# Kernel optimization log

Measured on AMD Instinct MI355X. Metric: run time of the kernel, lower is better.

## Reference

```python
import jax, jax.numpy as jnp
import numpy as np
from jax import lax

EPS = 1e-06
QP_ITERS = 500  # unrolled mirror-descent iterations for the simplex QP


def mlp_embed(x, W1, b1, W2, b2):
    # embedding_net: 2-layer MLP, [B, N, in_dim] -> [B, N, embed_dim]
    h = jax.nn.relu(jnp.einsum('bni,ih->bnh', x, W1) + b1)
    return jnp.einsum('bnh,hd->bnd', h, W2) + b2


def batch_svdd(emb, eps):
    # emb: [B, S, D].  SVDD dual QP per task:
    #   min_a  a^T K a - diag(K)^T a   s.t.  a >= 0, sum(a) = 1
    # (Q = 2K, p = -diag(K), G = -I, h = 0, A = 1^T, b = 1 in the torch QPFunction call)
    B, S, D = emb.shape
    K = jnp.einsum('bsd,btd->bst', emb, emb) + eps * jnp.eye(S, dtype=emb.dtype)
    kdiag = jnp.diagonal(K, axis1=-2, axis2=-1)  # [B, S]
    # Solve on the simplex with exponentiated-gradient (mirror descent with KL),
    # which converges to the unique QP optimum (K is PD after the eps jitter).
    # Per-task step size from the Gershgorin bound: eta <= 1 / (2 * ||K||_inf).
    eta = 1.0 / (2.0 * jnp.max(jnp.sum(jnp.abs(K), axis=-1), axis=-1, keepdims=True))  # [B,1]
    a0 = jnp.full((B, S), 1.0 / S, dtype=emb.dtype)

    def step(a, _):
        g = 2.0 * jnp.einsum('bst,bt->bs', K, a) - kdiag  # grad of a^T K a - kdiag^T a
        a = jax.nn.softmax(jnp.log(a + 1e-30) - eta * g, axis=-1)
        return a, None

    alphas, _ = lax.scan(step, a0, None, length=QP_ITERS)
    centers = jnp.einsum('bs,bsd->bd', alphas, emb)  # sum(alphas * inputs, dim=1)
    return centers


def setup_inputs() -> dict:
    key = jax.random.key(0)
    ks = jax.random.split(key, 4)
    tasks, shot, n_query, in_dim, hid, emb = 256, 32, 64, 1024, 2048, 512
    support_inputs = jax.random.normal(ks[0], (tasks, shot, in_dim), jnp.float32)
    query_inputs = jax.random.normal(ks[1], (tasks, n_query, in_dim), jnp.float32)
    W1 = jax.random.normal(ks[2], (in_dim, hid), jnp.float32) / np.sqrt(in_dim)
    b1 = jnp.zeros((hid,), jnp.float32)
    W2 = jax.random.normal(ks[3], (hid, emb), jnp.float32) / np.sqrt(hid)
    b2 = jnp.zeros((emb,), jnp.float32)
    return {'support_inputs': support_inputs, 'query_inputs': query_inputs,
            'W1': W1, 'b1': b1, 'W2': W2, 'b2': b2}


def reference(support_inputs, query_inputs, W1, b1, W2, b2):
    support_emb = mlp_embed(support_inputs, W1, b1, W2, b2)  # [B, S, D]
    centers = batch_svdd(support_emb, EPS)                   # [B, D]
    query_emb = mlp_embed(query_inputs, W1, b1, W2, b2)      # [B, Q, D]
    logits = -jnp.sum((centers[:, None, :] - query_emb) ** 2, axis=-1)  # [B, Q]
    return logits
```

## Files before the change

### kernel.cpp

```cpp
#include <hip/hip_runtime.h>
#include <hip/hip_bf16.h>

typedef __attribute__((ext_vector_type(8))) short bf16x8;
typedef __attribute__((ext_vector_type(4))) float f32x4;
typedef __attribute__((ext_vector_type(4))) unsigned short us4;

__device__ __forceinline__ unsigned short bf16_rne(float f) {
  unsigned u = __float_as_uint(f);
  unsigned r = u + 0x7fffu + ((u >> 16) & 1u);
  return (unsigned short)(r >> 16);
}

__device__ __forceinline__ void gload16(const void* g, void* l) {
  typedef const __attribute__((address_space(1))) unsigned int* gas;
  typedef __attribute__((address_space(3))) unsigned int* las;
  __builtin_amdgcn_global_load_lds((gas)g, (las)l, 16, 0, 0);
}

__device__ __forceinline__ float lane_f(float v, int l) {
  return __int_as_float(__builtin_amdgcn_readlane(__float_as_int(v), l));
}

template <int CTRL>
__device__ __forceinline__ float dpp_add(float x) {
  return x + __int_as_float(__builtin_amdgcn_update_dpp(0, __float_as_int(x), CTRL, 0xf, 0xf, true));
}

#define BAR() asm volatile("s_barrier" ::: "memory")
#define VMCNT0() asm volatile("s_waitcnt vmcnt(0)" ::: "memory")
#define LGKM4() asm volatile("s_waitcnt lgkmcnt(4)" ::: "memory")
#define LGKM0() asm volatile("s_waitcnt lgkmcnt(0)" ::: "memory")
#define SB() __builtin_amdgcn_sched_barrier(0)

__global__ __launch_bounds__(256) void castx(const float* __restrict__ sup,
                                             const float* __restrict__ qry,
                                             unsigned short* __restrict__ X) {
  const int stride = gridDim.x * blockDim.x;
  for (int i = blockIdx.x * blockDim.x + threadIdx.x; i < 6291456; i += stride) {
    float4 v = (i < 2097152) ? ((const float4*)sup)[i] : ((const float4*)qry)[i - 2097152];
    us4 o = { bf16_rne(v.x), bf16_rne(v.y), bf16_rne(v.z), bf16_rne(v.w) };
    *(us4*)(X + (size_t)i * 4) = o;
  }
}

__global__ __launch_bounds__(256) void transcast(const float* __restrict__ src,
                                                 unsigned short* __restrict__ dst,
                                                 int R, int C) {
  __shared__ float t[32][33];
  const int tx = threadIdx.x & 31, ty = threadIdx.x >> 5;
  const int c0 = blockIdx.x * 32, r0 = blockIdx.y * 32;
#pragma unroll
  for (int j = 0; j < 4; j++)
    t[ty + j * 8][tx] = src[(size_t)(r0 + ty + j * 8) * C + c0 + tx];
  __syncthreads();
#pragma unroll
  for (int j = 0; j < 4; j++)
    dst[(size_t)(c0 + ty + j * 8) * R + r0 + tx] = bf16_rne(t[tx][ty + j * 8]);
}

#define MFMA_Q(AO, BO, MOFF, NOFF)                                                  \
  __builtin_amdgcn_s_setprio(1);                                                    \
  _Pragma("unroll") for (int i_ = 0; i_ < 4; ++i_)                                  \
  _Pragma("unroll") for (int j_ = 0; j_ < 2; ++j_)                                  \
  _Pragma("unroll") for (int ks_ = 0; ks_ < 2; ++ks_)                               \
    acc[(MOFF) + i_][(NOFF) + j_] = __builtin_amdgcn_mfma_f32_16x16x32_bf16(        \
        AO[i_][ks_], BO[j_][ks_], acc[(MOFF) + i_][(NOFF) + j_], 0, 0, 0);          \
  __builtin_amdgcn_s_setprio(0);

#define RDA(KS, ACH, MH, I) \
  (*(const bf16x8*)(lsc + ((ACH) * 32768 + (MH) * 8192 + (I) * 2048) + ((KS) ? vA_1 : vA_0)))
#define RDB(KS, BCH, JI) \
  (*(const bf16x8*)(lsc + ((BCH) * 32768 + (JI) * 2048) + ((KS) ? vB_1 : vB_0)))

#define STG(GLP, CHOFF, HALF)                                                     \
  gload16((GLP) + (size_t)((HALF) * 128) * ld,                                    \
          (char*)ls + ((CHOFF) + (HALF) * 16384) + wid * 1024);                   \
  gload16((GLP) + (size_t)((HALF) * 128 + 64) * ld,                               \
          (char*)ls + ((CHOFF) + (HALF) * 16384 + 8192) + wid * 1024);

#define TILE(ACH, BCH, ASO, BSO, T)                                               \
  {                                                                               \
    VMCNT0();                                                                     \
    BAR();                                                                        \
    _Pragma("unroll") for (int i = 0; i < 4; ++i) {                               \
      afr[i][0] = RDA(0, ACH, 0, i); afr[i][1] = RDA(1, ACH, 0, i);               \
    }                                                                             \
    _Pragma("unroll") for (int j = 0; j < 2; ++j) {                               \
      bfr0[j][0] = RDB(0, BCH, j); bfr0[j][1] = RDB(1, BCH, j);                   \
    }                                                                             \
    _Pragma("unroll") for (int j = 0; j < 2; ++j) {                               \
      bfr1[j][0] = RDB(0, BCH, 2 + j); bfr1[j][1] = RDB(1, BCH, 2 + j);           \
    }                                                                             \
    const char* Ap_ = AgL + (size_t)(T) * 128;                                    \
    const char* Bp_ = BgL + (size_t)(T) * 128;                                    \
    STG(Ap_, ASO, 0); STG(Ap_, ASO, 1);                                           \
    STG(Bp_, BSO, 0); STG(Bp_, BSO, 1);                                           \
    LGKM4(); SB();                                                                \
    MFMA_Q(afr, bfr0, 0, 0);                                                      \
    LGKM0(); SB();                                                                \
    MFMA_Q(afr, bfr1, 0, 2);                                                      \
    _Pragma("unroll") for (int i = 0; i < 4; ++i) {                               \
      afr[i][0] = RDA(0, ACH, 1, i); afr[i][1] = RDA(1, ACH, 1, i);               \
    }                                                                             \
    LGKM0(); SB();                                                                \
    MFMA_Q(afr, bfr1, 4, 2);                                                      \
    MFMA_Q(afr, bfr0, 4, 0);                                                      \
  }

template <int ACT, int OUTBF>
__global__ __launch_bounds__(512) void gemm256(const unsigned short* __restrict__ A,
                                               const unsigned short* __restrict__ BT,
                                               const float* __restrict__ bias,
                                               void* __restrict__ Cout,
                                               int M, int N, int K) {
  __shared__ __attribute__((aligned(16))) short ls[4][16384];
  const int tid = threadIdx.x, lane = tid & 63, wid = tid >> 6;
  const int wm = wid >> 2, wn = wid & 3;
  const int l15 = lane & 15, lg = lane >> 4;

  int lin = blockIdx.y * gridDim.x + blockIdx.x;
  int nwg = gridDim.x * gridDim.y;
  int swz = (lin & 7) * (nwg >> 3) + (lin >> 3);
  int bx = swz % gridDim.x, by = swz / gridDim.x;
  const int m0 = by * 256, n0 = bx * 256;

  const size_t ld = (size_t)K * 2;
  const char* Ag = (const char*)A + (size_t)m0 * ld;
  const char* Bg = (const char*)BT + (size_t)n0 * ld;
  const int NT = K >> 6;
  const char* lsc = (const char*)ls;

  const int swz4 = (l15 & 7) << 4;
  const int bk0 = (l15 * 128 + lg * 16) ^ swz4;
  const int bk1 = (l15 * 128 + 64 + lg * 16) ^ swz4;
  const int vA_0 = bk0 + wm * 16384, vA_1 = bk1 + wm * 16384;
  const int vB_0 = bk0 + wn * 8192 + 65536, vB_1 = bk1 + wn * 8192 + 65536;

  const int srow = wid * 8 + (lane >> 3);
  const int kperm = ((lane & 7) ^ (lane >> 3)) << 4;
  const char* AgL = Ag + (size_t)srow * ld + kperm;
  const char* BgL = Bg + (size_t)srow * ld + kperm;

  f32x4 acc[8][4] = {};
  bf16x8 afr[4][2], bfr0[2][2], bfr1[2][2];

  STG(AgL, 0, 0); STG(AgL, 0, 1);
  STG(BgL, 65536, 0); STG(BgL, 65536, 1);

  for (int u = 0; u < NT; u += 2) {
    int t1 = u + 1;
    int t2 = u + 2; if (t2 >= NT) t2 = 0;
    TILE(0, 0, 32768, 98304, t1);
    TILE(1, 1, 0, 65536, t2);
  }

  float bv[4];
#pragma unroll
  for (int nf = 0; nf < 4; ++nf) bv[nf] = bias[n0 + wn * 64 + nf * 16 + l15];
#pragma unroll
  for (int mf = 0; mf < 8; ++mf) {
    int rbase = m0 + wm * 128 + mf * 16 + lg * 4;
#pragma unroll
    for (int nf = 0; nf < 4; ++nf) {
      int col = n0 + wn * 64 + nf * 16 + l15;
#pragma unroll
      for (int j = 0; j < 4; ++j) {
        float v = acc[mf][nf][j] + bv[nf];
        if (ACT) v = v > 0.f ? v : 0.f;
        size_t idx = (size_t)(rbase + j) * N + col;
        if (OUTBF) ((unsigned short*)Cout)[idx] = bf16_rne(v);
        else       ((float*)Cout)[idx] = v;
      }
    }
  }
}

template <int K>
__global__ __launch_bounds__(256, 2) void gemm2(const unsigned short* __restrict__ A,
                                                const unsigned short* __restrict__ BT,
                                                const float* __restrict__ bias,
                                                float* __restrict__ Cout,
                                                int N) {
  __shared__ __attribute__((aligned(16))) short ls[2][18432];
  const int tid = threadIdx.x, lane = tid & 63, wid = tid >> 6;
  const int l15 = lane & 15, lg = lane >> 4;

  int lin = blockIdx.x;
  int nwg = gridDim.x;
  int swz = (lin & 7) * (nwg >> 3) + (lin >> 3);
  const int m0 = swz * 64;

  constexpr size_t ldb = (size_t)K * 2;
  constexpr int NT = K >> 5;
  const char* Ag = (const char*)A + (size_t)m0 * ldb;
  const char* Bg = (const char*)BT;
  char* lsw = (char*)ls;
  const char* lsc = (const char*)ls;

  const int vb = l15 * 64 + ((lg ^ (l15 & 3)) << 4);

  const int kperm = ((lane & 3) ^ ((lane >> 2) & 3)) << 4;
  const char* AgL = Ag + (size_t)(wid * 16 + (lane >> 2)) * ldb + kperm;
  const char* BgL = Bg + (size_t)(wid * 128 + (lane >> 2)) * ldb + kperm;

  f32x4 acc[4][8] = {};
  bf16x8 afr[4], bfr[8];

  auto STAGE = [&](int buf, int t) {
    gload16(AgL + (size_t)t * 64, lsw + buf * 36864 + wid * 1024);
#pragma unroll
    for (int q = 0; q < 8; ++q)
      gload16(BgL + (size_t)(q * 16) * ldb + (size_t)t * 64,
              lsw + buf * 36864 + 4096 + wid * 8192 + q * 1024);
  };

  auto TILE2 = [&](int ch, int oc, int tst) {
    VMCNT0();
    BAR();
#pragma unroll
    for (int i = 0; i < 4; ++i)
      afr[i] = *(const bf16x8*)(lsc + ch * 36864 + i * 1024 + vb);
#pragma unroll
    for (int nf = 0; nf < 8; ++nf)
      bfr[nf] = *(const bf16x8*)(lsc + ch * 36864 + 4096 + wid * 8192 + nf * 1024 + vb);
    STAGE(oc, tst);
    __builtin_amdgcn_s_setprio(1);
#pragma unroll
    for (int nf = 0; nf < 8; ++nf)
#pragma unroll
      for (int i = 0; i < 4; ++i)
        acc[i][nf] = __builtin_amdgcn_mfma_f32_16x16x32_bf16(afr[i], bfr[nf],
                                                             acc[i][nf], 0, 0, 0);
    __builtin_amdgcn_s_setprio(0);
  };

  STAGE(0, 0);
  for (int u = 0; u < NT; u += 2) {
    int t2 = u + 2; if (t2 >= NT) t2 = 0;
    TILE2(0, 1, u + 1);
    TILE2(1, 0, t2);
  }

  float bv[8];
#pragma unroll
  for (int nf = 0; nf < 8; ++nf) bv[nf] = bias[wid * 128 + nf * 16 + l15];
#pragma unroll
  for (int i = 0; i < 4; ++i) {
    int rbase = m0 + i * 16 + lg * 4;
#pragma unroll
    for (int nf = 0; nf < 8; ++nf) {
      int col = wid * 128 + nf * 16 + l15;
#pragma unroll
      for (int j = 0; j < 4; ++j)
        Cout[(size_t)(rbase + j) * N + col] = acc[i][nf][j] + bv[nf];
    }
  }
}

__global__ __launch_bounds__(256) void makeK(const float* __restrict__ E,
                                             float* __restrict__ Km,
                                             float* __restrict__ eta2v) {
  __shared__ float es[32][512];
  const int b = blockIdx.x, tid = threadIdx.x;
  const float4* Eb = (const float4*)(E + (size_t)b * 32 * 512);
  float4* es4 = (float4*)&es[0][0];
  for (int i = tid; i < 32 * 128; i += 256) es4[i] = Eb[i];
  __syncthreads();

  const int s = tid >> 3, tq = tid & 7;
  const float4* rs4 = (const float4*)&es[s][0];
  const float4* rt0 = (const float4*)&es[tq * 4 + 0][0];
  const float4* rt1 = (const float4*)&es[tq * 4 + 1][0];
  const float4* rt2 = (const float4*)&es[tq * 4 + 2][0];
  const float4* rt3 = (const float4*)&es[tq * 4 + 3][0];
  float4 a0 = {0, 0, 0, 0}, a1 = {0, 0, 0, 0}, a2 = {0, 0, 0, 0}, a3 = {0, 0, 0, 0};
  for (int dd = 0; dd < 128; ++dd) {
    float4 av = rs4[dd];
    float4 b0 = rt0[dd], b1 = rt1[dd], b2 = rt2[dd], b3 = rt3[dd];
    a0.x = fmaf(av.x, b0.x, a0.x); a0.y = fmaf(av.y, b0.y, a0.y);
    a0.z = fmaf(av.z, b0.z, a0.z); a0.w = fmaf(av.w, b0.w, a0.w);
    a1.x = fmaf(av.x, b1.x, a1.x); a1.y = fmaf(av.y, b1.y, a1.y);
    a1.z = fmaf(av.z, b1.z, a1.z); a1.w = fmaf(av.w, b1.w, a1.w);
    a2.x = fmaf(av.x, b2.x, a2.x); a2.y = fmaf(av.y, b2.y, a2.y);
    a2.z = fmaf(av.z, b2.z, a2.z); a2.w = fmaf(av.w, b2.w, a2.w);
    a3.x = fmaf(av.x, b3.x, a3.x); a3.y = fmaf(av.y, b3.y, a3.y);
    a3.z = fmaf(av.z, b3.z, a3.z); a3.w = fmaf(av.w, b3.w, a3.w);
  }
  float kv[4] = { (a0.x + a0.y) + (a0.z + a0.w), (a1.x + a1.y) + (a1.z + a1.w),
                  (a2.x + a2.y) + (a2.z + a2.w), (a3.x + a3.y) + (a3.z + a3.w) };
  float p = 0.f;
#pragma unroll
  for (int j = 0; j < 4; j++) {
    if (s == tq * 4 + j) kv[j] += 1e-6f;
    p += fabsf(kv[j]);
    Km[(size_t)b * 1024 + s * 32 + tq * 4 + j] = kv[j];
  }
  p += __shfl_xor(p, 1); p += __shfl_xor(p, 2); p += __shfl_xor(p, 4);
  __syncthreads();
  float* rs = &es[0][0];
  if (tq == 0) rs[s] = p;
  __syncthreads();
  if (tid < 32) {
    float m = rs[tid];
    m = fmaxf(m, __shfl_xor(m, 1));
    m = fmaxf(m, __shfl_xor(m, 2));
    m = fmaxf(m, __shfl_xor(m, 4));
    m = fmaxf(m, __shfl_xor(m, 8));
    m = fmaxf(m, __shfl_xor(m, 16));
    if (tid == 0) eta2v[b] = 1.4426950408889634f / (2.0f * m);
  }
}

__global__ __launch_bounds__(256) void qp_kernel(const float* __restrict__ Km,
                                                 const float* __restrict__ eta2v,
                                                 float* __restrict__ alp) {
  __shared__ float wl[4][32];
  const int lane = threadIdx.x & 63, wid = threadIdx.x >> 6;
  const int b = blockIdx.x * 4 + wid;
  const int s = lane & 31, h = lane >> 5;
  const float* Kb = Km + (size_t)b * 1024;
  float kr[16];
#pragma unroll
  for (int i = 0; i < 4; i++) {
    float4 v = ((const float4*)(Kb + s * 32 + h * 16))[i];
    kr[i * 4 + 0] = v.x; kr[i * 4 + 1] = v.y; kr[i * 4 + 2] = v.z; kr[i * 4 + 3] = v.w;
  }
  const float kd = Kb[s * 33];
  const float eta2 = eta2v[b];
  const float c2p = fmaf(eta2, kd, 1.0f);
  const float m4n = -4.0f * eta2;
  const float4* wv = (const float4*)&wl[wid][h * 16];
  float w = 0.03125f;
  for (int it = 0; it < 500; ++it) {
    wl[wid][s] = w;
    float r = w;
    r = dpp_add<0x128>(r);
    r = dpp_add<0x124>(r);
    r = dpp_add<0x122>(r);
    r = dpp_add<0x121>(r);
    r = dpp_add<0x142>(r);
    r = dpp_add<0x143>(r);
    float R2 = __builtin_amdgcn_rcpf(lane_f(r, 63));
    float4 q0 = wv[0], q1 = wv[1], q2 = wv[2], q3 = wv[3];
    float c0 = 0.f, c1 = 0.f, c2 = 0.f, c3 = 0.f;
    c0 = fmaf(kr[0],  q0.x, c0); c0 = fmaf(kr[1],  q0.y, c0);
    c0 = fmaf(kr[2],  q0.z, c0); c0 = fmaf(kr[3],  q0.w, c0);
    c1 = fmaf(kr[4],  q1.x, c1); c1 = fmaf(kr[5],  q1.y, c1);
    c1 = fmaf(kr[6],  q1.z, c1); c1 = fmaf(kr[7],  q1.w, c1);
    c2 = fmaf(kr[8],  q2.x, c2); c2 = fmaf(kr[9],  q2.y, c2);
    c2 = fmaf(kr[10], q2.z, c2); c2 = fmaf(kr[11], q2.w, c2);
    c3 = fmaf(kr[12], q3.x, c3); c3 = fmaf(kr[13], q3.y, c3);
    c3 = fmaf(kr[14], q3.z, c3); c3 = fmaf(kr[15], q3.w, c3);
    float half = (c0 + c1) + (c2 + c3);
    float tK = half + __shfl_xor(half, 32);
    float z = fmaf(m4n * R2, tK, c2p);
    w = (w * R2) * __builtin_amdgcn_exp2f(z);
  }
  float r = w;
  r = dpp_add<0x128>(r);
  r = dpp_add<0x124>(r);
  r = dpp_add<0x122>(r);
  r = dpp_add<0x121>(r);
  r = dpp_add<0x142>(r);
  r = dpp_add<0x143>(r);
  float R2 = __builtin_amdgcn_rcpf(lane_f(r, 63));
  if (lane < 32) alp[(size_t)b * 32 + s] = 2.0f * w * R2;
}

__global__ __launch_bounds__(128) void centers_k(const float* __restrict__ alp,
                                                 const float* __restrict__ E,
                                                 float* __restrict__ ctr) {
  const int b = blockIdx.x, t = threadIdx.x;
  __shared__ float av[32];
  if (t < 32) av[t] = alp[(size_t)b * 32 + t];
  __syncthreads();
  const float4* Eb = (const float4*)(E + (size_t)b * 32 * 512);
  float4 c = {0, 0, 0, 0};
#pragma unroll 8
  for (int sIdx = 0; sIdx < 32; sIdx++) {
    float a = av[sIdx];
    float4 v = Eb[sIdx * 128 + t];
    c.x = fmaf(a, v.x, c.x); c.y = fmaf(a, v.y, c.y);
    c.z = fmaf(a, v.z, c.z); c.w = fmaf(a, v.w, c.w);
  }
  ((float4*)ctr)[b * 128 + t] = c;
}

__global__ __launch_bounds__(256) void logits_k(const float* __restrict__ ctr,
                                                const float* __restrict__ E,
                                                float* __restrict__ out) {
  const int b = blockIdx.x, lane = threadIdx.x & 63, w = threadIdx.x >> 6;
  const float4* C4 = (const float4*)(ctr + (size_t)b * 512);
  const float4 cA = C4[lane * 2], cB = C4[lane * 2 + 1];
  const float4* Q4 = (const float4*)(E + (size_t)(8192 + b * 64) * 512);
  for (int q = w; q < 64; q += 4) {
    float4 e0 = Q4[(size_t)q * 128 + lane * 2];
    float4 e1 = Q4[(size_t)q * 128 + lane * 2 + 1];
    float d, ss = 0.f;
    d = cA.x - e0.x; ss = fmaf(d, d, ss);
    d = cA.y - e0.y; ss = fmaf(d, d, ss);
    d = cA.z - e0.z; ss = fmaf(d, d, ss);
    d = cA.w - e0.w; ss = fmaf(d, d, ss);
    d = cB.x - e1.x; ss = fmaf(d, d, ss);
    d = cB.y - e1.y; ss = fmaf(d, d, ss);
    d = cB.z - e1.z; ss = fmaf(d, d, ss);
    d = cB.w - e1.w; ss = fmaf(d, d, ss);
    ss += __shfl_xor(ss, 1);  ss += __shfl_xor(ss, 2);  ss += __shfl_xor(ss, 4);
    ss += __shfl_xor(ss, 8);  ss += __shfl_xor(ss, 16); ss += __shfl_xor(ss, 32);
    if (lane == 0) out[b * 64 + q] = -ss;
  }
}

extern "C" void kernel_launch(void* const* d_in, const int* in_sizes, int n_in,
                              void* d_out, int out_size, void* d_ws, size_t ws_size,
                              hipStream_t stream) {
  const float* sup = (const float*)d_in[0];
  const float* qry = (const float*)d_in[1];
  const float* W1  = (const float*)d_in[2];
  const float* b1  = (const float*)d_in[3];
  const float* W2  = (const float*)d_in[4];
  const float* b2  = (const float*)d_in[5];
  float* out = (float*)d_out;

  char* ws = (char*)d_ws;
  unsigned short* H   = (unsigned short*)(ws);
  unsigned short* Xbf = (unsigned short*)(ws + 100663296);
  float* E    = (float*)(ws + 100663296);
  unsigned short* W1T = (unsigned short*)(ws + 150994944);
  unsigned short* W2T = (unsigned short*)(ws + 155189248);
  float* Km   = (float*)(ws + 157286400);
  float* eta2 = (float*)(ws + 158334976);
  float* alp  = (float*)(ws + 158336000);
  float* ctr  = (float*)(ws + 158368768);

  castx<<<dim3(4096), dim3(256), 0, stream>>>(sup, qry, Xbf);
  transcast<<<dim3(64, 32), dim3(256), 0, stream>>>(W1, W1T, 1024, 2048);
  transcast<<<dim3(16, 64), dim3(256), 0, stream>>>(W2, W2T, 2048, 512);
  gemm256<1, 1><<<dim3(8, 96), dim3(512), 0, stream>>>(Xbf, W1T, b1, (void*)H, 24576, 2048, 1024);
  gemm2<2048><<<dim3(384), dim3(256), 0, stream>>>(H, W2T, b2, E, 512);
  makeK<<<dim3(256), dim3(256), 0, stream>>>(E, Km, eta2);
  qp_kernel<<<dim3(64), dim3(256), 0, stream>>>(Km, eta2, alp);
  centers_k<<<dim3(256), dim3(128), 0, stream>>>(alp, E, ctr);
  logits_k<<<dim3(256), dim3(256), 0, stream>>>(ctr, E, out);
}
```

Measured before the change: 341.5 us.

## Rework gemm256 LDS fragment pipelining and reuse it for second MLP layer

Inside the gemm256 tile loop, the global-to-LDS prefetch is now issued before the LDS fragment reads. Both A halves are loaded into separate register sets (afl/afh) up front, with staged lgkmcnt waits so MFMAs can start while later reads are still in flight. The dedicated gemm2 kernel for the second MLP layer is removed, and that layer now runs through gemm256 with a 2x96 grid of 256x256 tiles. The cost is more fragment registers and only 192 workgroups for layer 2, down from 384, which may reduce occupancy and load balance on that GEMM.

```diff
diff --git a/kernel.cpp b/kernel.cpp
--- a/kernel.cpp
+++ b/kernel.cpp
@@ -28,7 +28,8 @@
 
 #define BAR() asm volatile("s_barrier" ::: "memory")
 #define VMCNT0() asm volatile("s_waitcnt vmcnt(0)" ::: "memory")
-#define LGKM4() asm volatile("s_waitcnt lgkmcnt(4)" ::: "memory")
+#define LGKM12() asm volatile("s_waitcnt lgkmcnt(12)" ::: "memory")
+#define LGKM8() asm volatile("s_waitcnt lgkmcnt(8)" ::: "memory")
 #define LGKM0() asm volatile("s_waitcnt lgkmcnt(0)" ::: "memory")
 #define SB() __builtin_amdgcn_sched_barrier(0)
 
@@ -82,29 +83,31 @@
   {                                                                               \
     VMCNT0();                                                                     \
     BAR();                                                                        \
+    const char* Ap_ = AgL + (size_t)(T) * 128;                                    \
+    const char* Bp_ = BgL + (size_t)(T) * 128;                                    \
+    STG(Ap_, ASO, 0); STG(Ap_, ASO, 1);                                           \
+    STG(Bp_, BSO, 0); STG(Bp_, BSO, 1);                                           \
     _Pragma("unroll") for (int i = 0; i < 4; ++i) {                               \
-      afr[i][0] = RDA(0, ACH, 0, i); afr[i][1] = RDA(1, ACH, 0, i);               \
+      afl[i][0] = RDA(0, ACH, 0, i); afl[i][1] = RDA(1, ACH, 0, i);               \
     }                                                                             \
     _Pragma("unroll") for (int j = 0; j < 2; ++j) {                               \
       bfr0[j][0] = RDB(0, BCH, j); bfr0[j][1] = RDB(1, BCH, j);                   \
     }                                                                             \
+    SB();                                                                         \
     _Pragma("unroll") for (int j = 0; j < 2; ++j) {                               \
       bfr1[j][0] = RDB(0, BCH, 2 + j); bfr1[j][1] = RDB(1, BCH, 2 + j);           \
     }                                                                             \
-    const char* Ap_ = AgL + (size_t)(T) * 128;                                    \
-    const char* Bp_ = BgL + (size_t)(T) * 128;                                    \
-    STG(Ap_, ASO, 0); STG(Ap_, ASO, 1);                                           \
-    STG(Bp_, BSO, 0); STG(Bp_, BSO, 1);                                           \
-    LGKM4(); SB();                                                                \
-    MFMA_Q(afr, bfr0, 0, 0);                                                      \
+    SB();                                                                         \
+    _Pragma("unroll") for (int i = 0; i < 4; ++i) {                               \
+      afh[i][0] = RDA(0, ACH, 1, i); afh[i][1] = RDA(1, ACH, 1, i);               \
+    }                                                                             \
+    LGKM12(); SB();                                                               \
+    MFMA_Q(afl, bfr0, 0, 0);                                                      \
+    LGKM8(); SB();                                                                \
+    MFMA_Q(afl, bfr1, 0, 2);                                                      \
     LGKM0(); SB();                                                                \
-    MFMA_Q(afr, bfr1, 0, 2);                                                      \
-    _Pragma("unroll") for (int i = 0; i < 4; ++i) {                               \
-      afr[i][0] = RDA(0, ACH, 1, i); afr[i][1] = RDA(1, ACH, 1, i);               \
-    }                                                                             \
-    LGKM0(); SB();                                                                \
-    MFMA_Q(afr, bfr1, 4, 2);                                                      \
-    MFMA_Q(afr, bfr0, 4, 0);                                                      \
+    MFMA_Q(afh, bfr1, 4, 2);                                                      \
+    MFMA_Q(afh, bfr0, 4, 0);                                                      \
   }
 
 template <int ACT, int OUTBF>
@@ -142,7 +145,7 @@
   const char* BgL = Bg + (size_t)srow * ld + kperm;
 
   f32x4 acc[8][4] = {};
-  bf16x8 afr[4][2], bfr0[2][2], bfr1[2][2];
+  bf16x8 afl[4][2], afh[4][2], bfr0[2][2], bfr1[2][2];
 
   STG(AgL, 0, 0); STG(AgL, 0, 1);
   STG(BgL, 65536, 0); STG(BgL, 65536, 1);
@@ -171,88 +174,6 @@
         if (OUTBF) ((unsigned short*)Cout)[idx] = bf16_rne(v);
         else       ((float*)Cout)[idx] = v;
       }
-    }
-  }
-}
-
-template <int K>
-__global__ __launch_bounds__(256, 2) void gemm2(const unsigned short* __restrict__ A,
-                                                const unsigned short* __restrict__ BT,
-                                                const float* __restrict__ bias,
-                                                float* __restrict__ Cout,
-                                                int N) {
-  __shared__ __attribute__((aligned(16))) short ls[2][18432];
-  const int tid = threadIdx.x, lane = tid & 63, wid = tid >> 6;
-  const int l15 = lane & 15, lg = lane >> 4;
-
-  int lin = blockIdx.x;
-  int nwg = gridDim.x;
-  int swz = (lin & 7) * (nwg >> 3) + (lin >> 3);
-  const int m0 = swz * 64;
-
-  constexpr size_t ldb = (size_t)K * 2;
-  constexpr int NT = K >> 5;
-  const char* Ag = (const char*)A + (size_t)m0 * ldb;
-  const char* Bg = (const char*)BT;
-  char* lsw = (char*)ls;
-  const char* lsc = (const char*)ls;
-
-  const int vb = l15 * 64 + ((lg ^ (l15 & 3)) << 4);
-
-  const int kperm = ((lane & 3) ^ ((lane >> 2) & 3)) << 4;
-  const char* AgL = Ag + (size_t)(wid * 16 + (lane >> 2)) * ldb + kperm;
-  const char* BgL = Bg + (size_t)(wid * 128 + (lane >> 2)) * ldb + kperm;
-
-  f32x4 acc[4][8] = {};
-  bf16x8 afr[4], bfr[8];
-
-  auto STAGE = [&](int buf, int t) {
-    gload16(AgL + (size_t)t * 64, lsw + buf * 36864 + wid * 1024);
-#pragma unroll
-    for (int q = 0; q < 8; ++q)
-      gload16(BgL + (size_t)(q * 16) * ldb + (size_t)t * 64,
-              lsw + buf * 36864 + 4096 + wid * 8192 + q * 1024);
-  };
-
-  auto TILE2 = [&](int ch, int oc, int tst) {
-    VMCNT0();
-    BAR();
-#pragma unroll
-    for (int i = 0; i < 4; ++i)
-      afr[i] = *(const bf16x8*)(lsc + ch * 36864 + i * 1024 + vb);
-#pragma unroll
-    for (int nf = 0; nf < 8; ++nf)
-      bfr[nf] = *(const bf16x8*)(lsc + ch * 36864 + 4096 + wid * 8192 + nf * 1024 + vb);
-    STAGE(oc, tst);
-    __builtin_amdgcn_s_setprio(1);
-#pragma unroll
-    for (int nf = 0; nf < 8; ++nf)
-#pragma unroll
-      for (int i = 0; i < 4; ++i)
-        acc[i][nf] = __builtin_amdgcn_mfma_f32_16x16x32_bf16(afr[i], bfr[nf],
-                                                             acc[i][nf], 0, 0, 0);
-    __builtin_amdgcn_s_setprio(0);
-  };
-
-  STAGE(0, 0);
-  for (int u = 0; u < NT; u += 2) {
-    int t2 = u + 2; if (t2 >= NT) t2 = 0;
-    TILE2(0, 1, u + 1);
-    TILE2(1, 0, t2);
-  }
-
-  float bv[8];
-#pragma unroll
-  for (int nf = 0; nf < 8; ++nf) bv[nf] = bias[wid * 128 + nf * 16 + l15];
-#pragma unroll
-  for (int i = 0; i < 4; ++i) {
-    int rbase = m0 + i * 16 + lg * 4;
-#pragma unroll
-    for (int nf = 0; nf < 8; ++nf) {
-      int col = wid * 128 + nf * 16 + l15;
-#pragma unroll
-      for (int j = 0; j < 4; ++j)
-        Cout[(size_t)(rbase + j) * N + col] = acc[i][nf][j] + bv[nf];
     }
   }
 }
@@ -437,7 +358,7 @@
   transcast<<<dim3(64, 32), dim3(256), 0, stream>>>(W1, W1T, 1024, 2048);
   transcast<<<dim3(16, 64), dim3(256), 0, stream>>>(W2, W2T, 2048, 512);
   gemm256<1, 1><<<dim3(8, 96), dim3(512), 0, stream>>>(Xbf, W1T, b1, (void*)H, 24576, 2048, 1024);
-  gemm2<2048><<<dim3(384), dim3(256), 0, stream>>>(H, W2T, b2, E, 512);
+  gemm256<0, 0><<<dim3(2, 96), dim3(512), 0, stream>>>(H, W2T, b2, (void*)E, 24576, 512, 2048);
   makeK<<<dim3(256), dim3(256), 0, stream>>>(E, Km, eta2);
   qp_kernel<<<dim3(64), dim3(256), 0, stream>>>(Km, eta2, alp);
   centers_k<<<dim3(256), dim3(128), 0, stream>>>(alp, E, ctr);
```

Measured after the change: 313.7 us. 1.09x faster.
